# Kernel optimization log

Hardware: AMD Instinct MI355X
Metric: run time of the kernel (lower is better)

The kernel has to match this reference:

```python
import jax, jax.numpy as jnp
import numpy as np

X_DIM = 2048
C_DIM = 2048
I_DIM = X_DIM + C_DIM


def setup_inputs() -> dict:
    key = jax.random.key(0)
    ks = jax.random.split(key, 11)
    s = 1.0 / np.sqrt(I_DIM)  # ~nn.Linear init scale
    return {
        "h": jax.random.normal(ks[0], (C_DIM,), jnp.float32),
        "c": jax.random.normal(ks[1], (C_DIM,), jnp.float32),
        "x": jax.random.normal(ks[2], (X_DIM,), jnp.float32),
        "wf": jax.random.normal(ks[3], (C_DIM, I_DIM), jnp.float32) * s,
        "bf": jax.random.normal(ks[4], (C_DIM,), jnp.float32) * s,
        "wi": jax.random.normal(ks[5], (C_DIM, I_DIM), jnp.float32) * s,
        "bi": jax.random.normal(ks[6], (C_DIM,), jnp.float32) * s,
        "wo": jax.random.normal(ks[7], (C_DIM, I_DIM), jnp.float32) * s,
        "bo": jax.random.normal(ks[8], (C_DIM,), jnp.float32) * s,
        "wc": jax.random.normal(ks[9], (C_DIM, I_DIM), jnp.float32) * s,
        "bc": jax.random.normal(ks[10], (C_DIM,), jnp.float32) * s,
    }


def reference(h, c, x, wf, bf, wi, bi, wo, bo, wc, bc):
    # i = cat(x, h)  -> [x_dim + c_dim]
    i = jnp.concatenate([x, h])
    # Fuse 4 gate GEMVs into one [4*c_dim, i_dim] GEMV.
    W = jnp.concatenate([wf, wi, wc, wo], axis=0)  # [4*C, I]
    b = jnp.concatenate([bf, bi, bc, bo])          # [4*C]
    g = W @ i + b
    ff = jax.nn.sigmoid(g[0 * C_DIM:1 * C_DIM])
    ii = jax.nn.sigmoid(g[1 * C_DIM:2 * C_DIM])
    cc = jnp.tanh(g[2 * C_DIM:3 * C_DIM])
    oo = jax.nn.sigmoid(g[3 * C_DIM:4 * C_DIM])
    c_new = ff * c + ii * cc
    h_new = jnp.tanh(c_new) * oo
    return (c_new, h_new)
```

## Files before the change

kernel.cpp:

```cpp
#include <hip/hip_runtime.h>
#include <math.h>

#define C_DIMK 2048
#define I_DIMK 4096
#define NV4    (I_DIMK / 4)

__global__ __launch_bounds__(256, 4) void lstm_fused_kernel(
    const float* __restrict__ h, const float* __restrict__ c,
    const float* __restrict__ x,
    const float* __restrict__ wf, const float* __restrict__ bf,
    const float* __restrict__ wi, const float* __restrict__ bi,
    const float* __restrict__ wo, const float* __restrict__ bo,
    const float* __restrict__ wc, const float* __restrict__ bc,
    float* __restrict__ out)
{
    __shared__ float4 xs[NV4];
    const int r    = blockIdx.x;
    const int t    = threadIdx.x;
    const int wave = t >> 6;
    const int lane = t & 63;

    const float* W = (wave == 0) ? wf : (wave == 1) ? wi : (wave == 2) ? wc : wo;
    const float4* Wrow = reinterpret_cast<const float4*>(W) + (size_t)r * NV4;

    float4 w[16];
    #pragma unroll
    for (int j = 0; j < 16; ++j) w[j] = Wrow[j * 64 + lane];

    const float4* X4 = reinterpret_cast<const float4*>(x);
    const float4* H4 = reinterpret_cast<const float4*>(h);
    #pragma unroll
    for (int j = 0; j < 4; ++j) {
        const int idx = j * 256 + t;
        xs[idx] = (idx < 512) ? X4[idx] : H4[idx - 512];
    }
    __syncthreads();

    float a0 = 0.f, a1 = 0.f, a2 = 0.f, a3 = 0.f;
    #pragma unroll
    for (int j = 0; j < 16; ++j) {
        const float4 xv = xs[j * 64 + lane];
        const float4 wv = w[j];
        float d = wv.x * xv.x;
        d = fmaf(wv.y, xv.y, d);
        d = fmaf(wv.z, xv.z, d);
        d = fmaf(wv.w, xv.w, d);
        switch (j & 3) {
            case 0: a0 += d; break;
            case 1: a1 += d; break;
            case 2: a2 += d; break;
            default: a3 += d; break;
        }
    }
    float sum = (a0 + a1) + (a2 + a3);

    #pragma unroll
    for (int off = 32; off > 0; off >>= 1)
        sum += __shfl_down(sum, off, 64);

    __shared__ float partial[4];
    if (lane == 0) partial[wave] = sum;
    __syncthreads();

    if (t == 0) {
        const float gf = partial[0] + bf[r];
        const float gi = partial[1] + bi[r];
        const float gc = partial[2] + bc[r];
        const float go = partial[3] + bo[r];
        const float ff = 1.0f / (1.0f + __expf(-gf));
        const float ig = 1.0f / (1.0f + __expf(-gi));
        const float cc = tanhf(gc);
        const float oo = 1.0f / (1.0f + __expf(-go));
        const float cn = fmaf(ff, c[r], ig * cc);
        const float hn = tanhf(cn) * oo;
        out[r]          = cn;
        out[C_DIMK + r] = hn;
    }
}

extern "C" void kernel_launch(void* const* d_in, const int* in_sizes, int n_in,
                              void* d_out, int out_size, void* d_ws, size_t ws_size,
                              hipStream_t stream) {
    const float* h  = (const float*)d_in[0];
    const float* c  = (const float*)d_in[1];
    const float* x  = (const float*)d_in[2];
    const float* wf = (const float*)d_in[3];
    const float* bf = (const float*)d_in[4];
    const float* wi = (const float*)d_in[5];
    const float* bi = (const float*)d_in[6];
    const float* wo = (const float*)d_in[7];
    const float* bo = (const float*)d_in[8];
    const float* wc = (const float*)d_in[9];
    const float* bc = (const float*)d_in[10];
    float* out = (float*)d_out;

    lstm_fused_kernel<<<C_DIMK, 256, 0, stream>>>(
        h, c, x, wf, bf, wi, bi, wo, bo, wc, bc, out);
}
```

Baseline: 161.8 us.

## Split each gate row across all waves with nontemporal loads and register-held inputs

Instead of one wave per gate reading a whole 4096-float row, all 256 threads now split every gate's row, each thread loading 4 float4s from each of the four weight matrices with nontemporal loads. The x/h input vector is read straight into registers, which removes the shared-memory staging and one barrier. Four shuffle reductions per wave plus a cross-wave sum in thread 0 replace the single reduction. The goal is wider, streaming-friendly HBM access without polluting the cache, at the cost of more shuffle work per block.

```diff
diff --git a/kernel.cpp b/kernel.cpp
--- a/kernel.cpp
+++ b/kernel.cpp
@@ -2,8 +2,8 @@
 #include <math.h>
 
 #define C_DIMK 2048
-#define I_DIMK 4096
-#define NV4    (I_DIMK / 4)
+
+typedef float f32x4 __attribute__((ext_vector_type(4)));
 
 __global__ __launch_bounds__(256, 4) void lstm_fused_kernel(
     const float* __restrict__ h, const float* __restrict__ c,
@@ -14,59 +14,80 @@
     const float* __restrict__ wc, const float* __restrict__ bc,
     float* __restrict__ out)
 {
-    __shared__ float4 xs[NV4];
     const int r    = blockIdx.x;
     const int t    = threadIdx.x;
     const int wave = t >> 6;
     const int lane = t & 63;
 
-    const float* W = (wave == 0) ? wf : (wave == 1) ? wi : (wave == 2) ? wc : wo;
-    const float4* Wrow = reinterpret_cast<const float4*>(W) + (size_t)r * NV4;
+    const f32x4* X4 = reinterpret_cast<const f32x4*>(x);
+    const f32x4* H4 = reinterpret_cast<const f32x4*>(h);
+    f32x4 xv[4];
+    xv[0] = X4[t];
+    xv[1] = X4[256 + t];
+    xv[2] = H4[t];
+    xv[3] = H4[256 + t];
 
-    float4 w[16];
+    const f32x4* W4[4];
+    W4[0] = reinterpret_cast<const f32x4*>(wf) + (size_t)r * 1024;
+    W4[1] = reinterpret_cast<const f32x4*>(wi) + (size_t)r * 1024;
+    W4[2] = reinterpret_cast<const f32x4*>(wc) + (size_t)r * 1024;
+    W4[3] = reinterpret_cast<const f32x4*>(wo) + (size_t)r * 1024;
+
+    f32x4 wv0[4], wv1[4], wv2[4], wv3[4];
     #pragma unroll
-    for (int j = 0; j < 16; ++j) w[j] = Wrow[j * 64 + lane];
+    for (int j = 0; j < 4; ++j) wv0[j] = __builtin_nontemporal_load(&W4[0][j * 256 + t]);
+    #pragma unroll
+    for (int j = 0; j < 4; ++j) wv1[j] = __builtin_nontemporal_load(&W4[1][j * 256 + t]);
+    #pragma unroll
+    for (int j = 0; j < 4; ++j) wv2[j] = __builtin_nontemporal_load(&W4[2][j * 256 + t]);
+    #pragma unroll
+    for (int j = 0; j < 4; ++j) wv3[j] = __builtin_nontemporal_load(&W4[3][j * 256 + t]);
+    __builtin_amdgcn_sched_barrier(0);
 
-    const float4* X4 = reinterpret_cast<const float4*>(x);
-    const float4* H4 = reinterpret_cast<const float4*>(h);
+    float g[4];
     #pragma unroll
-    for (int j = 0; j < 4; ++j) {
-        const int idx = j * 256 + t;
-        xs[idx] = (idx < 512) ? X4[idx] : H4[idx - 512];
+    for (int k = 0; k < 4; ++k) {
+        const f32x4* wv = (k == 0) ? wv0 : (k == 1) ? wv1 : (k == 2) ? wv2 : wv3;
+        float d0 = wv[0].x * xv[0].x;
+        d0 = fmaf(wv[0].y, xv[0].y, d0);
+        d0 = fmaf(wv[0].z, xv[0].z, d0);
+        d0 = fmaf(wv[0].w, xv[0].w, d0);
+        float d1 = wv[1].x * xv[1].x;
+        d1 = fmaf(wv[1].y, xv[1].y, d1);
+        d1 = fmaf(wv[1].z, xv[1].z, d1);
+        d1 = fmaf(wv[1].w, xv[1].w, d1);
+        float d2 = wv[2].x * xv[2].x;
+        d2 = fmaf(wv[2].y, xv[2].y, d2);
+        d2 = fmaf(wv[2].z, xv[2].z, d2);
+        d2 = fmaf(wv[2].w, xv[2].w, d2);
+        float d3 = wv[3].x * xv[3].x;
+        d3 = fmaf(wv[3].y, xv[3].y, d3);
+        d3 = fmaf(wv[3].z, xv[3].z, d3);
+        d3 = fmaf(wv[3].w, xv[3].w, d3);
+        g[k] = (d0 + d1) + (d2 + d3);
+    }
+
+    #pragma unroll
+    for (int k = 0; k < 4; ++k) {
+        #pragma unroll
+        for (int off = 32; off > 0; off >>= 1)
+            g[k] += __shfl_down(g[k], off, 64);
+    }
+
+    __shared__ float partial[4][4];
+    if (lane == 0) {
+        partial[wave][0] = g[0];
+        partial[wave][1] = g[1];
+        partial[wave][2] = g[2];
+        partial[wave][3] = g[3];
     }
     __syncthreads();
 
-    float a0 = 0.f, a1 = 0.f, a2 = 0.f, a3 = 0.f;
-    #pragma unroll
-    for (int j = 0; j < 16; ++j) {
-        const float4 xv = xs[j * 64 + lane];
-        const float4 wv = w[j];
-        float d = wv.x * xv.x;
-        d = fmaf(wv.y, xv.y, d);
-        d = fmaf(wv.z, xv.z, d);
-        d = fmaf(wv.w, xv.w, d);
-        switch (j & 3) {
-            case 0: a0 += d; break;
-            case 1: a1 += d; break;
-            case 2: a2 += d; break;
-            default: a3 += d; break;
-        }
-    }
-    float sum = (a0 + a1) + (a2 + a3);
-
-    #pragma unroll
-    for (int off = 32; off > 0; off >>= 1)
-        sum += __shfl_down(sum, off, 64);
-
-    __shared__ float partial[4];
-    if (lane == 0) partial[wave] = sum;
-    __syncthreads();
-
     if (t == 0) {
-        const float gf = partial[0] + bf[r];
-        const float gi = partial[1] + bi[r];
-        const float gc = partial[2] + bc[r];
-        const float go = partial[3] + bo[r];
+        const float gf = partial[0][0] + partial[1][0] + partial[2][0] + partial[3][0] + bf[r];
+        const float gi = partial[0][1] + partial[1][1] + partial[2][1] + partial[3][1] + bi[r];
+        const float gc = partial[0][2] + partial[1][2] + partial[2][2] + partial[3][2] + bc[r];
+        const float go = partial[0][3] + partial[1][3] + partial[2][3] + partial[3][3] + bo[r];
         const float ff = 1.0f / (1.0f + __expf(-gf));
         const float ig = 1.0f / (1.0f + __expf(-gi));
         const float cc = tanhf(gc);
```

Result: faster. 156.3 us (-3.4%).

## Process four rows per block with double-buffered nontemporal weight loads

Applied to the files above, without the earlier changes.

Each block now computes four output rows instead of one, so the x/h staging into shared memory is amortised over four rows and the grid shrinks to 512 blocks. Weight rows are loaded with nontemporal loads into two register buffers in a ping-pong pattern, separated by scheduling barriers, so the next row's loads are in flight while the current row's dot product runs. This raises register pressure (launch bounds lowered to 2 blocks per SIMD) and gives fewer blocks to spread across CUs.

```diff
diff --git a/kernel.cpp b/kernel.cpp
--- a/kernel.cpp
+++ b/kernel.cpp
@@ -2,10 +2,35 @@
 #include <math.h>
 
 #define C_DIMK 2048
-#define I_DIMK 4096
-#define NV4    (I_DIMK / 4)
 
-__global__ __launch_bounds__(256, 4) void lstm_fused_kernel(
+typedef float f32x4 __attribute__((ext_vector_type(4)));
+
+
+#define ISSUE_ROW(buf, rowptr)                                         \
+  _Pragma("unroll")                                                    \
+  for (int j = 0; j < 16; ++j)                                         \
+    buf[j] = __builtin_nontemporal_load(&(rowptr)[j * 64 + lane]);
+
+#define DOT_ROW(buf, acc)                                              \
+  {                                                                    \
+    float d0 = 0.f, d1 = 0.f, d2 = 0.f, d3 = 0.f;                      \
+    _Pragma("unroll")                                                  \
+    for (int j = 0; j < 16; ++j) {                                     \
+      const f32x4 xvj = xs[j * 64 + lane];                             \
+      const f32x4 wv = buf[j];                                         \
+      float d = wv.x * xvj.x;                                          \
+      d = fmaf(wv.y, xvj.y, d);                                        \
+      d = fmaf(wv.z, xvj.z, d);                                        \
+      d = fmaf(wv.w, xvj.w, d);                                        \
+      if ((j & 3) == 0) d0 += d;                                       \
+      else if ((j & 3) == 1) d1 += d;                                  \
+      else if ((j & 3) == 2) d2 += d;                                  \
+      else d3 += d;                                                    \
+    }                                                                  \
+    acc = (d0 + d1) + (d2 + d3);                                       \
+  }
+
+__global__ __launch_bounds__(256, 2) void lstm_fused_kernel(
     const float* __restrict__ h, const float* __restrict__ c,
     const float* __restrict__ x,
     const float* __restrict__ wf, const float* __restrict__ bf,
@@ -14,59 +39,71 @@
     const float* __restrict__ wc, const float* __restrict__ bc,
     float* __restrict__ out)
 {
-    __shared__ float4 xs[NV4];
-    const int r    = blockIdx.x;
+    __shared__ f32x4 xs[1024];
+    __shared__ float partial[4][4];
+
     const int t    = threadIdx.x;
     const int wave = t >> 6;
     const int lane = t & 63;
+    const int r0   = blockIdx.x * 4;
 
-    const float* W = (wave == 0) ? wf : (wave == 1) ? wi : (wave == 2) ? wc : wo;
-    const float4* Wrow = reinterpret_cast<const float4*>(W) + (size_t)r * NV4;
-
-    float4 w[16];
+    const f32x4* X4 = reinterpret_cast<const f32x4*>(x);
+    const f32x4* H4 = reinterpret_cast<const f32x4*>(h);
     #pragma unroll
-    for (int j = 0; j < 16; ++j) w[j] = Wrow[j * 64 + lane];
-
-    const float4* X4 = reinterpret_cast<const float4*>(x);
-    const float4* H4 = reinterpret_cast<const float4*>(h);
-    #pragma unroll
-    for (int j = 0; j < 4; ++j) {
-        const int idx = j * 256 + t;
+    for (int k = 0; k < 4; ++k) {
+        const int idx = k * 256 + t;
         xs[idx] = (idx < 512) ? X4[idx] : H4[idx - 512];
     }
     __syncthreads();
 
-    float a0 = 0.f, a1 = 0.f, a2 = 0.f, a3 = 0.f;
-    #pragma unroll
-    for (int j = 0; j < 16; ++j) {
-        const float4 xv = xs[j * 64 + lane];
-        const float4 wv = w[j];
-        float d = wv.x * xv.x;
-        d = fmaf(wv.y, xv.y, d);
-        d = fmaf(wv.z, xv.z, d);
-        d = fmaf(wv.w, xv.w, d);
-        switch (j & 3) {
-            case 0: a0 += d; break;
-            case 1: a1 += d; break;
-            case 2: a2 += d; break;
-            default: a3 += d; break;
-        }
-    }
-    float sum = (a0 + a1) + (a2 + a3);
+    const float* W = (wave == 0) ? wf : (wave == 1) ? wi : (wave == 2) ? wc : wo;
+    const f32x4* Wm = reinterpret_cast<const f32x4*>(W);
+    const f32x4* row0 = Wm + (size_t)(r0 + 0) * 1024;
+    const f32x4* row1 = Wm + (size_t)(r0 + 1) * 1024;
+    const f32x4* row2 = Wm + (size_t)(r0 + 2) * 1024;
+    const f32x4* row3 = Wm + (size_t)(r0 + 3) * 1024;
+
+    f32x4 bufA[16], bufB[16];
+    float s0, s1, s2, s3;
+
+    ISSUE_ROW(bufA, row0);
+    __builtin_amdgcn_sched_barrier(0);
+    ISSUE_ROW(bufB, row1);
+    __builtin_amdgcn_sched_barrier(0);
+    DOT_ROW(bufA, s0);
+    __builtin_amdgcn_sched_barrier(0);
+    ISSUE_ROW(bufA, row2);
+    __builtin_amdgcn_sched_barrier(0);
+    DOT_ROW(bufB, s1);
+    __builtin_amdgcn_sched_barrier(0);
+    ISSUE_ROW(bufB, row3);
+    __builtin_amdgcn_sched_barrier(0);
+    DOT_ROW(bufA, s2);
+    __builtin_amdgcn_sched_barrier(0);
+    DOT_ROW(bufB, s3);
 
     #pragma unroll
-    for (int off = 32; off > 0; off >>= 1)
-        sum += __shfl_down(sum, off, 64);
+    for (int off = 32; off > 0; off >>= 1) {
+        s0 += __shfl_down(s0, off, 64);
+        s1 += __shfl_down(s1, off, 64);
+        s2 += __shfl_down(s2, off, 64);
+        s3 += __shfl_down(s3, off, 64);
+    }
 
-    __shared__ float partial[4];
-    if (lane == 0) partial[wave] = sum;
+    if (lane == 0) {
+        partial[wave][0] = s0;
+        partial[wave][1] = s1;
+        partial[wave][2] = s2;
+        partial[wave][3] = s3;
+    }
     __syncthreads();
 
-    if (t == 0) {
-        const float gf = partial[0] + bf[r];
-        const float gi = partial[1] + bi[r];
-        const float gc = partial[2] + bc[r];
-        const float go = partial[3] + bo[r];
+    if (t < 4) {
+        const int r = r0 + t;
+        const float gf = partial[0][t] + bf[r];
+        const float gi = partial[1][t] + bi[r];
+        const float gc = partial[2][t] + bc[r];
+        const float go = partial[3][t] + bo[r];
         const float ff = 1.0f / (1.0f + __expf(-gf));
         const float ig = 1.0f / (1.0f + __expf(-gi));
         const float cc = tanhf(gc);
@@ -94,6 +131,6 @@
     const float* bc = (const float*)d_in[10];
     float* out = (float*)d_out;
 
-    lstm_fused_kernel<<<C_DIMK, 256, 0, stream>>>(
+    lstm_fused_kernel<<<512, 256, 0, stream>>>(
         h, c, x, wf, bf, wi, bi, wo, bo, wc, bc, out);
 }
```

Result: slower. 177.2 us (+9.5%).
